# Kernel optimization log

Measured on AMD Instinct MI355X. Metric: run time of the kernel, lower is better.

## Reference

```python
import jax, jax.numpy as jnp
import numpy as np

N = 50000   # nodes
E = 800000  # edges (avg degree 16)
G = 256     # graphs in batch
IN = 64; H = 128; K = 8; C = 10; L = 3
TAU = 1.0


def _bn(x, g, b, eps=1e-5):
    # BatchNorm1d training-mode forward: batch stats over the row dim.
    m = x.mean(0)
    v = x.var(0)
    return (x - m) * jax.lax.rsqrt(v + eps) * g + b


def _ln(x, g, b, eps=1e-5):
    m = x.mean(-1, keepdims=True)
    v = x.var(-1, keepdims=True)
    return (x - m) * jax.lax.rsqrt(v + eps) * g + b


def setup_inputs() -> dict:
    key = jax.random.key(0)
    ks = jax.random.split(key, 16)
    p = lambda k, shape: jax.random.normal(k, shape, jnp.float32) * 0.05
    u = jax.random.uniform(ks[2], (N, K), minval=1e-10, maxval=1.0)
    return {
        "x": jax.random.normal(ks[0], (N, IN), jnp.float32),
        "edge_index": jax.random.randint(ks[1], (2, E), 0, N, dtype=jnp.int32),
        "batch": (jnp.arange(N, dtype=jnp.int32) * G) // N,  # sorted, all graphs present
        "gumbel": -jnp.log(-jnp.log(u)),  # fixed Gumbel(0,1) noise
        "inp_w": p(ks[3], (IN, H)), "inp_b": jnp.zeros(H),
        "elin_w": p(ks[4], (L, 1, H)), "elin_b": jnp.zeros((L, H)),
        "mlp1_w": p(ks[5], (L, H, H)), "mlp1_b": jnp.zeros((L, H)),
        "mlpbn_g": jnp.ones((L, H)), "mlpbn_b": jnp.zeros((L, H)),
        "mlp2_w": p(ks[6], (L, H, H)), "mlp2_b": jnp.zeros((L, H)),
        "bn_g": jnp.ones((L, H)), "bn_b": jnp.zeros((L, H)),
        "bh1_w": p(ks[7], (H, H // 2)), "bh1_b": jnp.zeros(H // 2),
        "bh2_w": p(ks[8], (H // 2, K)), "bh2_b": jnp.zeros(K),
        "bm_w": p(ks[9], (H, H)), "bm_b": jnp.zeros(H),
        "ln_g": jnp.ones(H), "ln_b": jnp.zeros(H),
        "clf1_w": p(ks[10], (2 * H, H)), "clf1_b": jnp.zeros(H),
        "clfbn_g": jnp.ones(H), "clfbn_b": jnp.zeros(H),
        "clf2_w": p(ks[11], (H, C)), "clf2_b": jnp.zeros(C),
    }


def reference(x, edge_index, batch, gumbel, inp_w, inp_b, elin_w, elin_b,
              mlp1_w, mlp1_b, mlpbn_g, mlpbn_b, mlp2_w, mlp2_b, bn_g, bn_b,
              bh1_w, bh1_b, bh2_w, bh2_b, bm_w, bm_b, ln_g, ln_b,
              clf1_w, clf1_b, clfbn_g, clfbn_b, clf2_w, clf2_b):
    src, dst = edge_index[0], edge_index[1]
    h = x @ inp_w + inp_b  # [N,H]
    for l in range(L):  # GINEConv stack (eps=0, dummy edge attr = ones[E,1])
        e_emb = elin_w[l][0] + elin_b[l]          # ones @ W + b -> single [H] vector
        msg = jax.nn.relu(h[src] + e_emb)          # gather + add, [E,H]
        aggr = jax.ops.segment_sum(msg, dst, num_segments=N)  # scatter-add
        z = h + aggr                               # (1+eps)*x + aggr, eps=0
        z = jax.nn.relu(_bn(z @ mlp1_w[l] + mlp1_b[l], mlpbn_g[l], mlpbn_b[l]))
        z = z @ mlp2_w[l] + mlp2_b[l]
        h = jax.nn.relu(_bn(z, bn_g[l], bn_b[l]))
    # blob assignment via gumbel-softmax (soft)
    logits = jax.nn.relu(h @ bh1_w + bh1_b) @ bh2_w + bh2_b  # [N,K]
    assign = jax.nn.softmax((logits + gumbel) / TAU, axis=-1)
    counts = jax.ops.segment_sum(jnp.ones((N,), h.dtype), batch, num_segments=G)
    gmean = jax.ops.segment_sum(h, batch, num_segments=G) / counts[:, None]  # [G,H]
    # per-graph weighted blob pooling, vectorized over graphs via segment_sum
    num = jax.ops.segment_sum(assign[:, :, None] * h[:, None, :], batch, num_segments=G)  # [G,K,H]
    den = jax.ops.segment_sum(assign, batch, num_segments=G)  # [G,K]
    blobs = num / (den[:, :, None] + 1e-8)
    blobs = _ln(jax.nn.relu(blobs @ bm_w + bm_b), ln_g, ln_b)
    blob_emb = blobs.max(axis=1)  # [G,H]
    z = jnp.concatenate([gmean, blob_emb], axis=-1)  # [G,2H]
    z = jax.nn.relu(_bn(z @ clf1_w + clf1_b, clfbn_g, clfbn_b))
    return z @ clf2_w + clf2_b  # [G,C]
```

## Files before the change

kernel.cpp:

```cpp
#include <hip/hip_runtime.h>
#include <hip/hip_bf16.h>


#define HH 128
typedef unsigned short u16;
typedef unsigned int u32;
typedef __attribute__((ext_vector_type(8))) short bf16x8;
typedef __attribute__((ext_vector_type(4))) float f32x4;

__device__ __forceinline__ void atomAddF(float* p, float v) { unsafeAtomicAdd(p, v); }

__device__ __forceinline__ u16 f2bf(float f) {
    u32 u = __float_as_uint(f);
    u += 0x7fffu + ((u >> 16) & 1u);
    return (u16)(u >> 16);
}
__device__ __forceinline__ float bf2f_lo(u32 u) { return __uint_as_float(u << 16); }
__device__ __forceinline__ float bf2f_hi(u32 u) { return __uint_as_float(u & 0xffff0000u); }
__device__ __forceinline__ void split2(float v, u16& hi, u16& lo) {
    u16 h_ = f2bf(v);
    float hf = __uint_as_float(((u32)h_) << 16);
    hi = h_;
    lo = f2bf(v - hf);
}
__device__ __forceinline__ u32 swz(u32 row, u32 kByte, u32 strideB) {
    return (row * strideB + kByte) ^ ((row & 7u) << 4);
}

#define WTOT (8192 + 6 * 16384)

__global__ void k_prep(const float* __restrict__ inp_w, const float* __restrict__ m1,
                       const float* __restrict__ m2, u16* __restrict__ Whi,
                       u16* __restrict__ Wlo) {
    int b = blockIdx.x;
    int t = threadIdx.x;
    if (b == 0) {
        for (int idx = t; idx < 128 * 64; idx += 256) {
            int c = idx >> 6, k = idx & 63;
            u16 hi, lo;
            split2(inp_w[k * 128 + c], hi, lo);
            Whi[idx] = hi; Wlo[idx] = lo;
        }
    } else {
        const float* W = (b <= 3) ? m1 + (size_t)(b - 1) * 16384
                                  : m2 + (size_t)(b - 4) * 16384;
        u16* dh = Whi + 8192 + (size_t)(b - 1) * 16384;
        u16* dl = Wlo + 8192 + (size_t)(b - 1) * 16384;
        for (int idx = t; idx < 16384; idx += 256) {
            int c = idx >> 7, k = idx & 127;
            u16 hi, lo;
            split2(W[k * 128 + c], hi, lo);
            dh[idx] = hi; dl[idx] = lo;
        }
    }
}

__global__ void k_split(const float* __restrict__ x, u16* __restrict__ xhi,
                        u16* __restrict__ xlo, int total4) {
    int i = blockIdx.x * 256 + threadIdx.x;
    if (i >= total4) return;
    float4 v = *(const float4*)(x + (size_t)i * 4);
    u16 h0, h1, h2, h3, l0, l1, l2, l3;
    split2(v.x, h0, l0); split2(v.y, h1, l1);
    split2(v.z, h2, l2); split2(v.w, h3, l3);
    uint2 ph = {(u32)h0 | ((u32)h1 << 16), (u32)h2 | ((u32)h3 << 16)};
    uint2 pl = {(u32)l0 | ((u32)l1 << 16), (u32)l2 | ((u32)l3 << 16)};
    *(uint2*)(xhi + (size_t)i * 4) = ph;
    *(uint2*)(xlo + (size_t)i * 4) = pl;
}

__global__ void k_hist(const int* __restrict__ ei, int* __restrict__ deg, int E) {
    int i4 = blockIdx.x * 256 + threadIdx.x;
    int e0 = i4 * 4;
    if (e0 + 3 < E) {
        int4 d = *(const int4*)(ei + E + e0);
        atomicAdd(&deg[d.x], 1);
        atomicAdd(&deg[d.y], 1);
        atomicAdd(&deg[d.z], 1);
        atomicAdd(&deg[d.w], 1);
    } else {
        for (int e = e0; e < E; e++) atomicAdd(&deg[ei[E + e]], 1);
    }
}

__global__ void k_bsum(const int* __restrict__ deg, int* __restrict__ bsum, int N) {
    int t = threadIdx.x;
    int i = blockIdx.x * 256 + t;
    int v = (i < N) ? deg[i] : 0;
    for (int o = 32; o; o >>= 1) v += __shfl_down(v, o);
    __shared__ int ws_[4];
    if ((t & 63) == 0) ws_[t >> 6] = v;
    __syncthreads();
    if (t == 0) bsum[blockIdx.x] = ws_[0] + ws_[1] + ws_[2] + ws_[3];
}

__global__ void k_scan1(const int* __restrict__ bsum, int* __restrict__ boff,
                        int* __restrict__ rowptrN, int nch) {
    int t = threadIdx.x;
    int v = (t < nch) ? bsum[t] : 0;
    int l = t & 63, w = t >> 6;
    int sv = v;
    for (int o = 1; o < 64; o <<= 1) { int u = __shfl_up(sv, o); if (l >= o) sv += u; }
    __shared__ int wsum[4];
    if (l == 63) wsum[w] = sv;
    __syncthreads();
    int add = 0;
    for (int j = 0; j < w; j++) add += wsum[j];
    if (t < nch) boff[t] = sv - v + add;
    if (t == nch - 1) *rowptrN = sv + add;
}

__global__ void k_scan2(const int* __restrict__ deg, const int* __restrict__ boff,
                        int* __restrict__ rowptr, int* __restrict__ cursor, int N) {
    int b = blockIdx.x, t = threadIdx.x, i = b * 256 + t;
    int v = (i < N) ? deg[i] : 0;
    int l = t & 63, w = t >> 6;
    int sv = v;
    for (int o = 1; o < 64; o <<= 1) { int u = __shfl_up(sv, o); if (l >= o) sv += u; }
    __shared__ int wsum[4];
    if (l == 63) wsum[w] = sv;
    __syncthreads();
    int add = boff[b];
    for (int j = 0; j < w; j++) add += wsum[j];
    if (i < N) { int e = sv - v + add; rowptr[i] = e; cursor[i] = e; }
}

__global__ void k_fill(const int* __restrict__ ei, int* __restrict__ cursor,
                       int* __restrict__ col, int E) {
    int i4 = blockIdx.x * 256 + threadIdx.x;
    int e0 = i4 * 4;
    if (e0 + 3 < E) {
        int4 s = *(const int4*)(ei + e0);
        int4 d = *(const int4*)(ei + E + e0);
        int p0 = atomicAdd(&cursor[d.x], 1);
        int p1 = atomicAdd(&cursor[d.y], 1);
        int p2 = atomicAdd(&cursor[d.z], 1);
        int p3 = atomicAdd(&cursor[d.w], 1);
        col[p0] = s.x;
        col[p1] = s.y;
        col[p2] = s.z;
        col[p3] = s.w;
    } else {
        for (int e = e0; e < E; e++) {
            int pos = atomicAdd(&cursor[ei[E + e]], 1);
            col[pos] = ei[e];
        }
    }
}

template <int KD, int MODE, bool STATS, bool BOUT>
__global__ __launch_bounds__(512) void k_mgemm(
    const float* __restrict__ inf, const u16* __restrict__ inhi,
    const u16* __restrict__ inlo, const u16* __restrict__ Whi,
    const u16* __restrict__ Wlo, const float* __restrict__ bias,
    const float* __restrict__ statsIn, const float* __restrict__ gamma,
    const float* __restrict__ beta, float invN,
    float* __restrict__ out, u16* __restrict__ outb,
    float* __restrict__ statsOut, int Nrows, int ntiles) {
    __shared__ u16 s_Ahi[128 * KD];
    __shared__ u16 s_Alo[128 * KD];
    __shared__ u16 s_Bhi[128 * KD];
    __shared__ u16 s_Blo[128 * KD];
    __shared__ float s_red[2][8][128];
    __shared__ float s_sc[128], s_sh[128];
    const int t = threadIdx.x;
    constexpr u32 STR = KD * 2;
    constexpr int KCB = KD / 8;
    constexpr int KCF = KD / 4;
    constexpr int NAU = (128 * KCB) / 512;
    constexpr int NAF = (128 * KCF) / 512;
    constexpr int NB  = (128 * KCB) / 512;

#pragma unroll
    for (int i = 0; i < NB; i++) {
        int idx = i * 512 + t;
        int c = idx / KCB, kc = idx % KCB;
        u32 off = swz(c, kc * 16, STR);
        *(uint4*)((char*)s_Bhi + off) = *(const uint4*)(Whi + (size_t)c * KD + kc * 8);
        *(uint4*)((char*)s_Blo + off) = *(const uint4*)(Wlo + (size_t)c * KD + kc * 8);
    }
    if (MODE == 1 && t < 128) {
        float m = statsIn[t] * invN;
        float var = statsIn[128 + t] * invN - m * m;
        float s = gamma[t] * rsqrtf(var + 1e-5f);
        s_sc[t] = s;
        s_sh[t] = beta[t] - m * s;
    }
    __syncthreads();

    float4 rf[MODE == 1 ? NAF : 1];
    uint4 rh[MODE == 2 ? NAU : 1], rl[MODE == 2 ? NAU : 1];
    int tile = blockIdx.x;
    if (tile < ntiles) {
        if (MODE == 1) {
#pragma unroll
            for (int i = 0; i < NAF; i++) {
                int idx = i * 512 + t;
                int r = idx / KCF, kc = idx % KCF;
                int gr = tile * 128 + r;
                rf[i] = (gr < Nrows) ? *(const float4*)(inf + (size_t)gr * KD + kc * 4)
                                     : (float4){0.f, 0.f, 0.f, 0.f};
            }
        } else {
#pragma unroll
            for (int i = 0; i < NAU; i++) {
                int idx = i * 512 + t;
                int r = idx / KCB, kc = idx % KCB;
                int gr = tile * 128 + r;
                if (gr < Nrows) {
                    rh[i] = *(const uint4*)(inhi + (size_t)gr * KD + kc * 8);
                    rl[i] = *(const uint4*)(inlo + (size_t)gr * KD + kc * 8);
                } else {
                    rh[i] = (uint4){0, 0, 0, 0};
                    rl[i] = (uint4){0, 0, 0, 0};
                }
            }
        }
    }

    const int l = t & 63, w = t >> 6;
    const int c0 = l & 15;
    const u32 kOffB = (u32)(l >> 4) * 16u;
    const u32 rA_row = w * 16 + c0;

    for (; tile < ntiles; tile += gridDim.x) {
        if (MODE == 1) {
#pragma unroll
            for (int i = 0; i < NAF; i++) {
                int idx = i * 512 + t;
                int r = idx / KCF, kc = idx % KCF;
                float4 v = rf[i];
                int k0 = kc * 4;
                v.x = fmaxf(v.x * s_sc[k0 + 0] + s_sh[k0 + 0], 0.f);
                v.y = fmaxf(v.y * s_sc[k0 + 1] + s_sh[k0 + 1], 0.f);
                v.z = fmaxf(v.z * s_sc[k0 + 2] + s_sh[k0 + 2], 0.f);
                v.w = fmaxf(v.w * s_sc[k0 + 3] + s_sh[k0 + 3], 0.f);
                u16 h0, h1, h2, h3, l0, l1, l2, l3;
                split2(v.x, h0, l0); split2(v.y, h1, l1);
                split2(v.z, h2, l2); split2(v.w, h3, l3);
                uint2 ph = {(u32)h0 | ((u32)h1 << 16), (u32)h2 | ((u32)h3 << 16)};
                uint2 pl = {(u32)l0 | ((u32)l1 << 16), (u32)l2 | ((u32)l3 << 16)};
                u32 off = swz(r, kc * 8, STR);
                *(uint2*)((char*)s_Ahi + off) = ph;
                *(uint2*)((char*)s_Alo + off) = pl;
            }
        } else {
#pragma unroll
            for (int i = 0; i < NAU; i++) {
                int idx = i * 512 + t;
                int r = idx / KCB, kc = idx % KCB;
                u32 off = swz(r, kc * 16, STR);
                *(uint4*)((char*)s_Ahi + off) = rh[i];
                *(uint4*)((char*)s_Alo + off) = rl[i];
            }
        }
        __syncthreads();

        int nxt = tile + gridDim.x;
        if (nxt < ntiles) {
            if (MODE == 1) {
#pragma unroll
                for (int i = 0; i < NAF; i++) {
                    int idx = i * 512 + t;
                    int r = idx / KCF, kc = idx % KCF;
                    int gr = nxt * 128 + r;
                    rf[i] = (gr < Nrows) ? *(const float4*)(inf + (size_t)gr * KD + kc * 4)
                                         : (float4){0.f, 0.f, 0.f, 0.f};
                }
            } else {
#pragma unroll
                for (int i = 0; i < NAU; i++) {
                    int idx = i * 512 + t;
                    int r = idx / KCB, kc = idx % KCB;
                    int gr = nxt * 128 + r;
                    if (gr < Nrows) {
                        rh[i] = *(const uint4*)(inhi + (size_t)gr * KD + kc * 8);
                        rl[i] = *(const uint4*)(inlo + (size_t)gr * KD + kc * 8);
                    } else {
                        rh[i] = (uint4){0, 0, 0, 0};
                        rl[i] = (uint4){0, 0, 0, 0};
                    }
                }
            }
        }

        f32x4 acc[8];
#pragma unroll
        for (int n = 0; n < 8; n++) acc[n] = (f32x4){0.f, 0.f, 0.f, 0.f};
#pragma unroll
        for (int kk = 0; kk < KD / 32; kk++) {
            u32 kb = kk * 64 + kOffB;
            bf16x8 ah = *(const bf16x8*)((char*)s_Ahi + swz(rA_row, kb, STR));
            bf16x8 al = *(const bf16x8*)((char*)s_Alo + swz(rA_row, kb, STR));
#pragma unroll
            for (int n = 0; n < 8; n++) {
                u32 ob = swz(n * 16 + c0, kb, STR);
                bf16x8 bh = *(const bf16x8*)((char*)s_Bhi + ob);
                bf16x8 bl = *(const bf16x8*)((char*)s_Blo + ob);
                acc[n] = __builtin_amdgcn_mfma_f32_16x16x32_bf16(ah, bh, acc[n], 0, 0, 0);
                acc[n] = __builtin_amdgcn_mfma_f32_16x16x32_bf16(al, bh, acc[n], 0, 0, 0);
                acc[n] = __builtin_amdgcn_mfma_f32_16x16x32_bf16(ah, bl, acc[n], 0, 0, 0);
            }
        }

        const int rbase = tile * 128 + w * 16 + ((l >> 4) << 2);
#pragma unroll
        for (int n = 0; n < 8; n++) {
            const int colc = n * 16 + c0;
            const float bv = bias[colc];
            float s = 0.f, q = 0.f;
#pragma unroll
            for (int j = 0; j < 4; j++) {
                int gr = rbase + j;
                if (gr < Nrows) {
                    float v = acc[n][j] + bv;
                    out[(size_t)gr * HH + colc] = v;
                    if (BOUT) outb[(size_t)gr * HH + colc] = f2bf(v);
                    s += v;
                    q += v * v;
                }
            }
            if (STATS) {
                s += __shfl_xor(s, 16); s += __shfl_xor(s, 32);
                q += __shfl_xor(q, 16); q += __shfl_xor(q, 32);
                if (l < 16) {
                    s_red[0][w][n * 16 + l] = s;
                    s_red[1][w][n * 16 + l] = q;
                }
            }
        }
        __syncthreads();
        if (STATS && t < 128) {
            float S = 0.f, Q = 0.f;
#pragma unroll
            for (int ww = 0; ww < 8; ww++) { S += s_red[0][ww][t]; Q += s_red[1][ww][t]; }
            atomAddF(&statsOut[t], S);
            atomAddF(&statsOut[HH + t], Q);
        }
    }
}

__global__ __launch_bounds__(256) void k_gather(
    const u16* __restrict__ hb, const float* __restrict__ h,
    const int* __restrict__ rowptr, const int* __restrict__ col,
    const float* __restrict__ ew, const float* __restrict__ eb,
    u16* __restrict__ zhi, u16* __restrict__ zlo, int N) {
    __shared__ float2 s_part[3][64];
    const int node = blockIdx.x;
    const int wv = threadIdx.x >> 6;
    const int lane = threadIdx.x & 63;
    const int c2 = lane * 2;
    const float2 ee = {ew[c2] + eb[c2], ew[c2 + 1] + eb[c2 + 1]};
    const int s = rowptr[node], eend = rowptr[node + 1];
    float2 acc = {0.f, 0.f};
    int e = s + wv;
    for (; e + 12 < eend; e += 16) {
        int s0 = col[e], s1 = col[e + 4], s2 = col[e + 8], s3 = col[e + 12];
        u32 u0 = *(const u32*)(hb + (size_t)s0 * HH + c2);
        u32 u1 = *(const u32*)(hb + (size_t)s1 * HH + c2);
        u32 u2 = *(const u32*)(hb + (size_t)s2 * HH + c2);
        u32 u3 = *(const u32*)(hb + (size_t)s3 * HH + c2);
        acc.x += fmaxf(bf2f_lo(u0) + ee.x, 0.f) + fmaxf(bf2f_lo(u1) + ee.x, 0.f) +
                 fmaxf(bf2f_lo(u2) + ee.x, 0.f) + fmaxf(bf2f_lo(u3) + ee.x, 0.f);
        acc.y += fmaxf(bf2f_hi(u0) + ee.y, 0.f) + fmaxf(bf2f_hi(u1) + ee.y, 0.f) +
                 fmaxf(bf2f_hi(u2) + ee.y, 0.f) + fmaxf(bf2f_hi(u3) + ee.y, 0.f);
    }
    for (; e < eend; e += 4) {
        u32 u0 = *(const u32*)(hb + (size_t)col[e] * HH + c2);
        acc.x += fmaxf(bf2f_lo(u0) + ee.x, 0.f);
        acc.y += fmaxf(bf2f_hi(u0) + ee.y, 0.f);
    }
    if (wv) s_part[wv - 1][lane] = acc;
    __syncthreads();
    if (wv == 0) {
        float2 p0 = s_part[0][lane], p1 = s_part[1][lane], p2 = s_part[2][lane];
        const float2 hn = *(const float2*)(h + (size_t)node * HH + c2);
        float zx = hn.x + acc.x + p0.x + p1.x + p2.x;
        float zy = hn.y + acc.y + p0.y + p1.y + p2.y;
        u16 h0, h1, l0, l1;
        split2(zx, h0, l0);
        split2(zy, h1, l1);
        *(u32*)(zhi + (size_t)node * HH + c2) = (u32)h0 | ((u32)h1 << 16);
        *(u32*)(zlo + (size_t)node * HH + c2) = (u32)l0 | ((u32)l1 << 16);
    }
}

__global__ void k_bnrelu(const float* __restrict__ t, const float* __restrict__ stats,
                         const float* __restrict__ g, const float* __restrict__ b,
                         float invN, float* __restrict__ h, u16* __restrict__ hb,
                         int total4) {
    int i = blockIdx.x * 256 + threadIdx.x;
    if (i >= total4) return;
    int c4 = (i & 31) << 2;
    float sc[4], sh[4];
#pragma unroll
    for (int j = 0; j < 4; j++) {
        float m = stats[c4 + j] * invN;
        float var = stats[128 + c4 + j] * invN - m * m;
        float s = g[c4 + j] * rsqrtf(var + 1e-5f);
        sc[j] = s;
        sh[j] = b[c4 + j] - m * s;
    }
    float4 v = *(const float4*)(t + (size_t)i * 4);
    float4 o;
    o.x = fmaxf(v.x * sc[0] + sh[0], 0.f);
    o.y = fmaxf(v.y * sc[1] + sh[1], 0.f);
    o.z = fmaxf(v.z * sc[2] + sh[2], 0.f);
    o.w = fmaxf(v.w * sc[3] + sh[3], 0.f);
    *(float4*)(h + (size_t)i * 4) = o;
    uint2 p = {(u32)f2bf(o.x) | ((u32)f2bf(o.y) << 16),
               (u32)f2bf(o.z) | ((u32)f2bf(o.w) << 16)};
    *(uint2*)(hb + (size_t)i * 4) = p;
}

__global__ __launch_bounds__(256) void k_assign(
    const float* __restrict__ h, const float* __restrict__ gum,
    const float* __restrict__ w1, const float* __restrict__ b1,
    const float* __restrict__ w2, const float* __restrict__ b2,
    float* __restrict__ assign, int N) {
    __shared__ float s_w1[128 * 64];
    __shared__ float s_w2[64 * 8];
    __shared__ float s_h[32][128];
    __shared__ float s_hid[32][64];
    const int t = threadIdx.x;
    const int n0 = blockIdx.x * 32;
    for (int i = t; i < 128 * 64; i += 256) s_w1[i] = w1[i];
    for (int i = t; i < 512; i += 256) s_w2[i] = w2[i];
    for (int i = t; i < 32 * 32; i += 256) {
        int r = i >> 5, c4 = (i & 31) << 2;
        int gn = n0 + r;
        float4 v = {0.f, 0.f, 0.f, 0.f};
        if (gn < N) v = *(const float4*)(h + (size_t)gn * HH + c4);
        *(float4*)(&s_h[r][c4]) = v;
    }
    __syncthreads();
    for (int o = t; o < 32 * 64; o += 256) {
        int nn = o >> 6, j = o & 63;
        float acc = b1[j];
        for (int k = 0; k < 128; k++) acc = fmaf(s_h[nn][k], s_w1[k * 64 + j], acc);
        s_hid[nn][j] = fmaxf(acc, 0.f);
    }
    __syncthreads();
    int nn = t >> 3, kk = t & 7;
    int gn = n0 + nn;
    float a = b2[kk];
    for (int j = 0; j < 64; j++) a = fmaf(s_hid[nn][j], s_w2[j * 8 + kk], a);
    if (gn < N) a += gum[(size_t)gn * 8 + kk];
    float m = a;
    m = fmaxf(m, __shfl_xor(m, 1));
    m = fmaxf(m, __shfl_xor(m, 2));
    m = fmaxf(m, __shfl_xor(m, 4));
    float e = expf(a - m);
    float s = e;
    s += __shfl_xor(s, 1); s += __shfl_xor(s, 2); s += __shfl_xor(s, 4);
    if (gn < N) assign[(size_t)gn * 8 + kk] = e / s;
}

__device__ __forceinline__ int lowerb(const int* __restrict__ arr, int n, int val) {
    int lo = 0, hi = n;
    while (lo < hi) {
        int mid = (lo + hi) >> 1;
        if (arr[mid] < val) lo = mid + 1;
        else hi = mid;
    }
    return lo;
}

__global__ __launch_bounds__(1024) void k_pool(
    const float* __restrict__ h, const float* __restrict__ assign,
    const int* __restrict__ batch, float* __restrict__ gmean,
    float* __restrict__ num, float* __restrict__ den, int N) {
    __shared__ float4 s_num[4][8][32];
    __shared__ float4 s_gm[4][32];
    __shared__ float s_den[4][8];
    const int g = blockIdx.x;
    const int t = threadIdx.x;
    const int ns = t >> 8;
    const int k = (t >> 5) & 7;
    const int lane = t & 31;
    const int c4 = lane << 2;
    const int start = lowerb(batch, N, g);
    const int end = lowerb(batch, N, g + 1);
    float4 an = {0.f, 0.f, 0.f, 0.f};
    float4 gm = {0.f, 0.f, 0.f, 0.f};
    float ad = 0.f;
    for (int n = start + ns; n < end; n += 4) {
        float a = assign[(size_t)n * 8 + k];
        const float4 hv = *(const float4*)(h + (size_t)n * HH + c4);
        an.x = fmaf(a, hv.x, an.x);
        an.y = fmaf(a, hv.y, an.y);
        an.z = fmaf(a, hv.z, an.z);
        an.w = fmaf(a, hv.w, an.w);
        if (k == 0) { gm.x += hv.x; gm.y += hv.y; gm.z += hv.z; gm.w += hv.w; }
        ad += a;
    }
    s_num[ns][k][lane] = an;
    if (k == 0) s_gm[ns][lane] = gm;
    if (lane == 0) s_den[ns][k] = ad;
    __syncthreads();
    if (t < 256) {
        float4 a0 = s_num[0][k][lane], a1 = s_num[1][k][lane];
        float4 a2 = s_num[2][k][lane], a3 = s_num[3][k][lane];
        float4 o = {a0.x + a1.x + a2.x + a3.x, a0.y + a1.y + a2.y + a3.y,
                    a0.z + a1.z + a2.z + a3.z, a0.w + a1.w + a2.w + a3.w};
        *(float4*)(num + ((size_t)g * 8 + k) * HH + c4) = o;
        if (t < 32) {
            float4 g0 = s_gm[0][lane], g1 = s_gm[1][lane];
            float4 g2 = s_gm[2][lane], g3 = s_gm[3][lane];
            int cnt = end - start;
            float inv = 1.f / (float)(cnt > 0 ? cnt : 1);
            float4 om = {(g0.x + g1.x + g2.x + g3.x) * inv,
                         (g0.y + g1.y + g2.y + g3.y) * inv,
                         (g0.z + g1.z + g2.z + g3.z) * inv,
                         (g0.w + g1.w + g2.w + g3.w) * inv};
            *(float4*)(gmean + (size_t)g * HH + c4) = om;
        }
        if (t < 8) den[(size_t)g * 8 + t] =
            s_den[0][t] + s_den[1][t] + s_den[2][t] + s_den[3][t];
    }
}

__global__ void k_blob(const float* __restrict__ num, const float* __restrict__ den,
                       const float* __restrict__ w, const float* __restrict__ b,
                       const float* __restrict__ lg, const float* __restrict__ lb,
                       float* __restrict__ blobs) {
    const int gk = blockIdx.x;
    const int c = threadIdx.x;
    __shared__ float srow[128];
    __shared__ float red[4];
    float d = den[gk] + 1e-8f;
    srow[c] = num[(size_t)gk * HH + c] / d;
    __syncthreads();
    float acc = b[c];
    for (int j = 0; j < 128; j++) acc = fmaf(srow[j], w[j * HH + c], acc);
    float y = fmaxf(acc, 0.f);
    float s = y, q = y * y;
    for (int off = 32; off > 0; off >>= 1) {
        s += __shfl_down(s, off);
        q += __shfl_down(q, off);
    }
    if ((c & 63) == 0) { red[(c >> 6) * 2] = s; red[(c >> 6) * 2 + 1] = q; }
    __syncthreads();
    float S = red[0] + red[2], Q = red[1] + red[3];
    float m = S * (1.f / 128.f);
    float var = Q * (1.f / 128.f) - m * m;
    blobs[(size_t)gk * HH + c] = (y - m) * rsqrtf(var + 1e-5f) * lg[c] + lb[c];
}

__global__ void k_clf1(const float* __restrict__ gmean, const float* __restrict__ blobs,
                       const float* __restrict__ w, const float* __restrict__ bias,
                       float* __restrict__ t4, float* __restrict__ stats) {
    int g = blockIdx.x;
    int c = threadIdx.x;
    __shared__ float s[256];
    float m = blobs[((size_t)g * 8) * HH + c];
#pragma unroll
    for (int k = 1; k < 8; k++) m = fmaxf(m, blobs[((size_t)g * 8 + k) * HH + c]);
    s[c] = gmean[(size_t)g * HH + c];
    s[128 + c] = m;
    __syncthreads();
    float acc = bias[c];
    for (int j = 0; j < 256; j++) acc = fmaf(s[j], w[j * HH + c], acc);
    t4[(size_t)g * HH + c] = acc;
    atomAddF(&stats[c], acc);
    atomAddF(&stats[HH + c], acc * acc);
}

__global__ void k_clf2(const float* __restrict__ t4, const float* __restrict__ stats,
                       const float* __restrict__ g_, const float* __restrict__ b_,
                       float invG, const float* __restrict__ w,
                       const float* __restrict__ bias, float* __restrict__ out) {
    int g = blockIdx.x;
    int t = threadIdx.x;
    __shared__ float s[128];
    float m = stats[t] * invG;
    float var = stats[128 + t] * invG - m * m;
    float sc = g_[t] * rsqrtf(var + 1e-5f);
    float sh = b_[t] - m * sc;
    s[t] = fmaxf(t4[(size_t)g * HH + t] * sc + sh, 0.f);
    __syncthreads();
    if (t < 10) {
        float acc = bias[t];
        for (int j = 0; j < 128; j++) acc = fmaf(s[j], w[j * 10 + t], acc);
        out[(size_t)g * 10 + t] = acc;
    }
}

extern "C" void kernel_launch(void* const* d_in, const int* in_sizes, int n_in,
                              void* d_out, int out_size, void* d_ws, size_t ws_size,
                              hipStream_t stream) {
    const float* x      = (const float*)d_in[0];
    const int*   ei     = (const int*)d_in[1];
    const int*   batch  = (const int*)d_in[2];
    const float* gumbel = (const float*)d_in[3];
    const float* inp_w  = (const float*)d_in[4];
    const float* inp_b  = (const float*)d_in[5];
    const float* elin_w = (const float*)d_in[6];
    const float* elin_b = (const float*)d_in[7];
    const float* mlp1_w = (const float*)d_in[8];
    const float* mlp1_b = (const float*)d_in[9];
    const float* mlpbn_g = (const float*)d_in[10];
    const float* mlpbn_b = (const float*)d_in[11];
    const float* mlp2_w = (const float*)d_in[12];
    const float* mlp2_b = (const float*)d_in[13];
    const float* bn_g   = (const float*)d_in[14];
    const float* bn_b   = (const float*)d_in[15];
    const float* bh1_w  = (const float*)d_in[16];
    const float* bh1_b  = (const float*)d_in[17];
    const float* bh2_w  = (const float*)d_in[18];
    const float* bh2_b  = (const float*)d_in[19];
    const float* bm_w   = (const float*)d_in[20];
    const float* bm_b   = (const float*)d_in[21];
    const float* ln_g   = (const float*)d_in[22];
    const float* ln_b   = (const float*)d_in[23];
    const float* clf1_w = (const float*)d_in[24];
    const float* clf1_b = (const float*)d_in[25];
    const float* clfbn_g = (const float*)d_in[26];
    const float* clfbn_b = (const float*)d_in[27];
    const float* clf2_w = (const float*)d_in[28];
    const float* clf2_b = (const float*)d_in[29];
    float* out = (float*)d_out;

    const int N = in_sizes[0] / 64;
    const int E = in_sizes[1] / 2;
    const int G = out_size / 10;

    float* ws = (float*)d_ws;
    float* h      = ws;
    float* zbuf   = h + (size_t)N * HH;
    float* t1     = zbuf + (size_t)N * HH;
    float* assign = t1 + (size_t)N * HH;
    float* gmean  = assign + (size_t)N * 8;
    float* num    = gmean + (size_t)G * HH;
    float* den    = num + (size_t)G * 8 * HH;
    float* blobs  = den + (size_t)G * 8;
    float* t4     = blobs + (size_t)G * 8 * HH;
    float* statsA = t4 + (size_t)G * HH;
    u16* Whi = (u16*)(statsA + 7 * 256);
    u16* Wlo = Whi + WTOT;
    int* rowptr = (int*)(Wlo + WTOT);
    int* cursor = rowptr + (N + 1);
    int* colidx = cursor + N;
    int* bsum   = colidx + E;
    int* boff   = bsum + 256;
    u16* hb  = (u16*)t1;
    u16* xhi = (u16*)zbuf;
    u16* xlo = xhi + (size_t)N * 64;
    u16* zhi = (u16*)zbuf;
    u16* zlo = zhi + (size_t)N * HH;
    float* t2 = zbuf;

    const dim3 B256(256), B128(128), B512(512), B1024(1024);
    const int ntiles = (N + 127) / 128;
    const int gg = ntiles < 256 ? ntiles : 256;
    const int nch = (N + 255) / 256;
    const int e4 = (E + 4 * 256 - 1) / (4 * 256);
    const float invN = 1.f / (float)N;
    const float invG = 1.f / (float)G;

    k_prep<<<7, B256, 0, stream>>>(inp_w, mlp1_w, mlp2_w, Whi, Wlo);
    hipMemsetAsync(cursor, 0, (size_t)N * sizeof(int), stream);
    hipMemsetAsync(statsA, 0, 7 * 256 * sizeof(float), stream);
    k_hist<<<e4, B256, 0, stream>>>(ei, cursor, E);
    k_bsum<<<nch, B256, 0, stream>>>(cursor, bsum, N);
    k_scan1<<<1, B256, 0, stream>>>(bsum, boff, rowptr + N, nch);
    k_scan2<<<nch, B256, 0, stream>>>(cursor, boff, rowptr, cursor, N);
    k_fill<<<e4, B256, 0, stream>>>(ei, cursor, colidx, E);
    k_split<<<(N * 16 + 255) / 256, B256, 0, stream>>>(x, xhi, xlo, N * 16);

    k_mgemm<64, 2, false, true><<<gg, B512, 0, stream>>>(
        nullptr, xhi, xlo, Whi, Wlo, inp_b, nullptr, nullptr, nullptr, 0.f,
        h, hb, nullptr, N, ntiles);

    for (int l = 0; l < 3; l++) {
        float* sa = statsA + (size_t)(2 * l) * 256;
        float* sb = statsA + (size_t)(2 * l + 1) * 256;
        k_gather<<<N, B256, 0, stream>>>(hb, h, rowptr, colidx,
                                         elin_w + l * HH, elin_b + l * HH,
                                         zhi, zlo, N);
        k_mgemm<128, 2, true, false><<<gg, B512, 0, stream>>>(
            nullptr, zhi, zlo, Whi + 8192 + (size_t)l * 16384,
            Wlo + 8192 + (size_t)l * 16384, mlp1_b + l * HH,
            nullptr, nullptr, nullptr, 0.f, t1, nullptr, sa, N, ntiles);
        k_mgemm<128, 1, true, false><<<gg, B512, 0, stream>>>(
            t1, nullptr, nullptr, Whi + 8192 + (size_t)(3 + l) * 16384,
            Wlo + 8192 + (size_t)(3 + l) * 16384, mlp2_b + l * HH,
            sa, mlpbn_g + l * HH, mlpbn_b + l * HH, invN, t2, nullptr, sb, N, ntiles);
        k_bnrelu<<<(N * 32 + 255) / 256, B256, 0, stream>>>(
            t2, sb, bn_g + l * HH, bn_b + l * HH, invN, h, hb, N * 32);
    }

    k_assign<<<(N + 31) / 32, B256, 0, stream>>>(h, gumbel, bh1_w, bh1_b, bh2_w, bh2_b, assign, N);
    k_pool<<<G, B1024, 0, stream>>>(h, assign, batch, gmean, num, den, N);
    k_blob<<<G * 8, B128, 0, stream>>>(num, den, bm_w, bm_b, ln_g, ln_b, blobs);
    float* sc_ = statsA + 6 * 256;
    k_clf1<<<G, B128, 0, stream>>>(gmean, blobs, clf1_w, clf1_b, t4, sc_);
    k_clf2<<<G, B128, 0, stream>>>(t4, sc_, clfbn_g, clfbn_b, invG, clf2_w, clf2_b, out);
}
```

Before: 572.4 us.

## Drop fp32 hidden-state writes between layers and pack two nodes per gather block

The gather kernel now takes the self term from the bf16 copy of h instead of the fp32 copy. This lets the input GEMM and the first two BN-ReLU passes skip writing the fp32 h, which removes full N×128 fp32 stores. The gather also processes two nodes per 256-thread block, with two waves per node, which halves the block count. The self term loses precision because it is rounded to bf16, and each node's edges are split across fewer waves.

```diff
diff --git a/kernel.cpp b/kernel.cpp
--- a/kernel.cpp
+++ b/kernel.cpp
@@ -148,7 +148,7 @@
     }
 }
 
-template <int KD, int MODE, bool STATS, bool BOUT>
+template <int KD, int MODE, bool STATS, bool FOUT, bool BOUT>
 __global__ __launch_bounds__(512) void k_mgemm(
     const float* __restrict__ inf, const u16* __restrict__ inhi,
     const u16* __restrict__ inlo, const u16* __restrict__ Whi,
@@ -314,7 +314,7 @@
                 int gr = rbase + j;
                 if (gr < Nrows) {
                     float v = acc[n][j] + bv;
-                    out[(size_t)gr * HH + colc] = v;
+                    if (FOUT) out[(size_t)gr * HH + colc] = v;
                     if (BOUT) outb[(size_t)gr * HH + colc] = f2bf(v);
                     s += v;
                     q += v * v;
@@ -341,42 +341,48 @@
 }
 
 __global__ __launch_bounds__(256) void k_gather(
-    const u16* __restrict__ hb, const float* __restrict__ h,
+    const u16* __restrict__ hb,
     const int* __restrict__ rowptr, const int* __restrict__ col,
     const float* __restrict__ ew, const float* __restrict__ eb,
     u16* __restrict__ zhi, u16* __restrict__ zlo, int N) {
-    __shared__ float2 s_part[3][64];
-    const int node = blockIdx.x;
+    __shared__ float2 s_part[2][64];
     const int wv = threadIdx.x >> 6;
     const int lane = threadIdx.x & 63;
+    const int node = blockIdx.x * 2 + (wv >> 1);
+    const int hf = wv & 1;
     const int c2 = lane * 2;
-    const float2 ee = {ew[c2] + eb[c2], ew[c2 + 1] + eb[c2 + 1]};
-    const int s = rowptr[node], eend = rowptr[node + 1];
     float2 acc = {0.f, 0.f};
-    int e = s + wv;
-    for (; e + 12 < eend; e += 16) {
-        int s0 = col[e], s1 = col[e + 4], s2 = col[e + 8], s3 = col[e + 12];
-        u32 u0 = *(const u32*)(hb + (size_t)s0 * HH + c2);
-        u32 u1 = *(const u32*)(hb + (size_t)s1 * HH + c2);
-        u32 u2 = *(const u32*)(hb + (size_t)s2 * HH + c2);
-        u32 u3 = *(const u32*)(hb + (size_t)s3 * HH + c2);
-        acc.x += fmaxf(bf2f_lo(u0) + ee.x, 0.f) + fmaxf(bf2f_lo(u1) + ee.x, 0.f) +
-                 fmaxf(bf2f_lo(u2) + ee.x, 0.f) + fmaxf(bf2f_lo(u3) + ee.x, 0.f);
-        acc.y += fmaxf(bf2f_hi(u0) + ee.y, 0.f) + fmaxf(bf2f_hi(u1) + ee.y, 0.f) +
-                 fmaxf(bf2f_hi(u2) + ee.y, 0.f) + fmaxf(bf2f_hi(u3) + ee.y, 0.f);
-    }
-    for (; e < eend; e += 4) {
-        u32 u0 = *(const u32*)(hb + (size_t)col[e] * HH + c2);
-        acc.x += fmaxf(bf2f_lo(u0) + ee.x, 0.f);
-        acc.y += fmaxf(bf2f_hi(u0) + ee.y, 0.f);
-    }
-    if (wv) s_part[wv - 1][lane] = acc;
-    __syncthreads();
-    if (wv == 0) {
-        float2 p0 = s_part[0][lane], p1 = s_part[1][lane], p2 = s_part[2][lane];
-        const float2 hn = *(const float2*)(h + (size_t)node * HH + c2);
-        float zx = hn.x + acc.x + p0.x + p1.x + p2.x;
-        float zy = hn.y + acc.y + p0.y + p1.y + p2.y;
+    const bool valid = node < N;
+    float2 ee = {0.f, 0.f};
+    if (valid) {
+        ee.x = ew[c2] + eb[c2];
+        ee.y = ew[c2 + 1] + eb[c2 + 1];
+        const int s = rowptr[node], eend = rowptr[node + 1];
+        int e = s + hf;
+        for (; e + 6 < eend; e += 8) {
+            int s0 = col[e], s1 = col[e + 2], s2 = col[e + 4], s3 = col[e + 6];
+            u32 u0 = *(const u32*)(hb + (size_t)s0 * HH + c2);
+            u32 u1 = *(const u32*)(hb + (size_t)s1 * HH + c2);
+            u32 u2 = *(const u32*)(hb + (size_t)s2 * HH + c2);
+            u32 u3 = *(const u32*)(hb + (size_t)s3 * HH + c2);
+            acc.x += fmaxf(bf2f_lo(u0) + ee.x, 0.f) + fmaxf(bf2f_lo(u1) + ee.x, 0.f) +
+                     fmaxf(bf2f_lo(u2) + ee.x, 0.f) + fmaxf(bf2f_lo(u3) + ee.x, 0.f);
+            acc.y += fmaxf(bf2f_hi(u0) + ee.y, 0.f) + fmaxf(bf2f_hi(u1) + ee.y, 0.f) +
+                     fmaxf(bf2f_hi(u2) + ee.y, 0.f) + fmaxf(bf2f_hi(u3) + ee.y, 0.f);
+        }
+        for (; e < eend; e += 2) {
+            u32 u0 = *(const u32*)(hb + (size_t)col[e] * HH + c2);
+            acc.x += fmaxf(bf2f_lo(u0) + ee.x, 0.f);
+            acc.y += fmaxf(bf2f_hi(u0) + ee.y, 0.f);
+        }
+    }
+    if (hf) s_part[wv >> 1][lane] = acc;
+    __syncthreads();
+    if (!hf && valid) {
+        float2 p = s_part[wv >> 1][lane];
+        u32 un = *(const u32*)(hb + (size_t)node * HH + c2);
+        float zx = bf2f_lo(un) + acc.x + p.x;
+        float zy = bf2f_hi(un) + acc.y + p.y;
         u16 h0, h1, l0, l1;
         split2(zx, h0, l0);
         split2(zy, h1, l1);
@@ -385,6 +391,7 @@
     }
 }
 
+template <bool WF>
 __global__ void k_bnrelu(const float* __restrict__ t, const float* __restrict__ stats,
                          const float* __restrict__ g, const float* __restrict__ b,
                          float invN, float* __restrict__ h, u16* __restrict__ hb,
@@ -407,7 +414,7 @@
     o.y = fmaxf(v.y * sc[1] + sh[1], 0.f);
     o.z = fmaxf(v.z * sc[2] + sh[2], 0.f);
     o.w = fmaxf(v.w * sc[3] + sh[3], 0.f);
-    *(float4*)(h + (size_t)i * 4) = o;
+    if (WF) *(float4*)(h + (size_t)i * 4) = o;
     uint2 p = {(u32)f2bf(o.x) | ((u32)f2bf(o.y) << 16),
                (u32)f2bf(o.z) | ((u32)f2bf(o.w) << 16)};
     *(uint2*)(hb + (size_t)i * 4) = p;
@@ -668,26 +675,30 @@
     k_fill<<<e4, B256, 0, stream>>>(ei, cursor, colidx, E);
     k_split<<<(N * 16 + 255) / 256, B256, 0, stream>>>(x, xhi, xlo, N * 16);
 
-    k_mgemm<64, 2, false, true><<<gg, B512, 0, stream>>>(
+    k_mgemm<64, 2, false, false, true><<<gg, B512, 0, stream>>>(
         nullptr, xhi, xlo, Whi, Wlo, inp_b, nullptr, nullptr, nullptr, 0.f,
-        h, hb, nullptr, N, ntiles);
+        nullptr, hb, nullptr, N, ntiles);
 
     for (int l = 0; l < 3; l++) {
         float* sa = statsA + (size_t)(2 * l) * 256;
         float* sb = statsA + (size_t)(2 * l + 1) * 256;
-        k_gather<<<N, B256, 0, stream>>>(hb, h, rowptr, colidx,
-                                         elin_w + l * HH, elin_b + l * HH,
-                                         zhi, zlo, N);
-        k_mgemm<128, 2, true, false><<<gg, B512, 0, stream>>>(
+        k_gather<<<(N + 1) / 2, B256, 0, stream>>>(hb, rowptr, colidx,
+                                                   elin_w + l * HH, elin_b + l * HH,
+                                                   zhi, zlo, N);
+        k_mgemm<128, 2, true, true, false><<<gg, B512, 0, stream>>>(
             nullptr, zhi, zlo, Whi + 8192 + (size_t)l * 16384,
             Wlo + 8192 + (size_t)l * 16384, mlp1_b + l * HH,
             nullptr, nullptr, nullptr, 0.f, t1, nullptr, sa, N, ntiles);
-        k_mgemm<128, 1, true, false><<<gg, B512, 0, stream>>>(
+        k_mgemm<128, 1, true, true, false><<<gg, B512, 0, stream>>>(
             t1, nullptr, nullptr, Whi + 8192 + (size_t)(3 + l) * 16384,
             Wlo + 8192 + (size_t)(3 + l) * 16384, mlp2_b + l * HH,
             sa, mlpbn_g + l * HH, mlpbn_b + l * HH, invN, t2, nullptr, sb, N, ntiles);
-        k_bnrelu<<<(N * 32 + 255) / 256, B256, 0, stream>>>(
-            t2, sb, bn_g + l * HH, bn_b + l * HH, invN, h, hb, N * 32);
+        if (l < 2)
+            k_bnrelu<false><<<(N * 32 + 255) / 256, B256, 0, stream>>>(
+                t2, sb, bn_g + l * HH, bn_b + l * HH, invN, nullptr, hb, N * 32);
+        else
+            k_bnrelu<true><<<(N * 32 + 255) / 256, B256, 0, stream>>>(
+                t2, sb, bn_g + l * HH, bn_b + l * HH, invN, h, hb, N * 32);
     }
 
     k_assign<<<(N + 31) / 32, B256, 0, stream>>>(h, gumbel, bh1_w, bh1_b, bh2_w, bh2_b, assign, N);
```

Result: faster. 524.6 us (-8.4%).
